# Optimization experiments

Hardware: AMD Instinct MI355X
Metric: run time of the kernel (lower is better)

## Reference

```python
import jax, jax.numpy as jnp
import numpy as np

N = 30000      # nodes
E = 480000     # edges (avg degree 16)
NF = 4         # n_field
NM = 8         # n_meshfield
H = 128        # hidden_size == latent_size
T = 4          # n_time
DEPTH_MID = 8  # depth-2 middle convs per GCNBlock
EPS = 1e-5     # PyG InstanceNorm eps
DT = 5 * (4.0 / 200)  # = 0.1, hard-coded in forward


def _glorot(k, shape):
    fan_in = shape[-2]
    return (jax.random.uniform(k, shape, jnp.float32, -1.0, 1.0) / np.sqrt(fan_in)).astype(jnp.float32)


def setup_inputs() -> dict:
    key = jax.random.key(0)
    ks = jax.random.split(key, 12)
    inp = {}
    inp['F_0'] = jax.random.normal(ks[0], (N, NF), jnp.float32)
    inp['edge_index'] = jax.random.randint(ks[1], (2, E), 0, N)
    inp['meshfield'] = jax.random.normal(ks[2], (N, NM), jnp.float32)
    inp['n_time'] = T
    # mesh_decriptor GCNBlock params (10 GCNConv layers)
    inp['mesh_W0'] = _glorot(ks[3], (NM, H)); inp['mesh_b0'] = jnp.zeros((H,), jnp.float32)
    inp['mesh_Wh'] = _glorot(ks[4], (DEPTH_MID, H, H)); inp['mesh_bh'] = jnp.zeros((DEPTH_MID, H), jnp.float32)
    inp['mesh_W9'] = _glorot(ks[5], (H, H)); inp['mesh_b9'] = jnp.zeros((H,), jnp.float32)
    # differentiator GCNBlock params; input dim = n_field + latent_size
    din = NF + H
    inp['diff_W0'] = _glorot(ks[6], (din, H)); inp['diff_b0'] = jnp.zeros((H,), jnp.float32)
    inp['diff_Wh'] = _glorot(ks[7], (DEPTH_MID, H, H)); inp['diff_bh'] = jnp.zeros((DEPTH_MID, H), jnp.float32)
    inp['diff_W9'] = _glorot(ks[8], (H, NF)); inp['diff_b9'] = jnp.zeros((NF,), jnp.float32)
    return inp


def _gcn_norm(edge_index, n):
    # PyG GCNConv: add self-loops, sym-normalize D^-1/2 (A+I) D^-1/2
    loops = jnp.arange(n)
    row = jnp.concatenate([edge_index[0], loops])
    col = jnp.concatenate([edge_index[1], loops])
    deg = jax.ops.segment_sum(jnp.ones_like(col, jnp.float32), col, num_segments=n)
    dinv = jnp.where(deg > 0, jax.lax.rsqrt(jnp.maximum(deg, 1.0)), 0.0)
    return row, col, dinv[row] * dinv[col]


def _conv(x, W, b, row, col, enorm, n):
    h = x @ W                                   # [n, out]
    m = h[row] * enorm[:, None]                 # gather + edge normalization
    return jax.ops.segment_sum(m, col, num_segments=n) + b  # scatter-add + bias


def _instance_norm(x):
    # single graph, affine=False: per-channel normalize over nodes
    m = x.mean(axis=0)
    v = x.var(axis=0)
    return (x - m) * jax.lax.rsqrt(v + EPS)


def _gcn_block(x, W0, b0, Wh, bh, W9, b9, row, col, enorm, n):
    x = _conv(x, W0, b0, row, col, enorm, n)
    x = _instance_norm(x)
    def body(c, wb):
        W, b = wb
        return _conv(jax.nn.relu(c), W, b, row, col, enorm, n), None
    x, _ = jax.lax.scan(body, x, (Wh, bh))
    return _conv(x, W9, b9, row, col, enorm, n)


def reference(F_0, edge_index, meshfield, n_time,
              mesh_W0, mesh_b0, mesh_Wh, mesh_bh, mesh_W9, mesh_b9,
              diff_W0, diff_b0, diff_Wh, diff_bh, diff_W9, diff_b9):
    n = F_0.shape[0]
    row, col, enorm = _gcn_norm(edge_index, n)
    mesh = jnp.tanh(_gcn_block(meshfield, mesh_W0, mesh_b0, mesh_Wh, mesh_bh,
                               mesh_W9, mesh_b9, row, col, enorm, n))

    def step(F_cur, _):
        x = jnp.concatenate([F_cur, mesh], axis=1)   # [n, n_field + latent]
        F_dot = jnp.tanh(_gcn_block(x, diff_W0, diff_b0, diff_Wh, diff_bh,
                                    diff_W9, diff_b9, row, col, enorm, n))
        F_next = jnp.tanh(F_cur + F_dot * DT)
        # original: F_current = F_next.detach()
        return jax.lax.stop_gradient(F_next), (F_next, F_dot)

    _, (Fs, F_dots) = jax.lax.scan(step, F_0, None, length=n_time)
    # [T, n, f] -> [n, T, f] to match torch.cat(..., dim=1)
    return jnp.transpose(Fs, (1, 0, 2)), jnp.transpose(F_dots, (1, 0, 2))
```

## Files before the change

### kernel.cpp

```cpp
#include <hip/hip_runtime.h>
#include <math.h>

typedef __attribute__((ext_vector_type(8))) short short8;
typedef __attribute__((ext_vector_type(4))) float f32x4;
typedef unsigned int uint;
typedef unsigned short ushort;

__device__ __forceinline__ ushort f2bf(float f) {
  union { float f; uint u; } v; v.f = f;
  uint u = v.u;
  uint r = (u + 0x7FFFu + ((u >> 16) & 1u)) >> 16;
  return (ushort)r;
}
__device__ __forceinline__ float bflo(uint u) { union { uint u; float f; } v; v.u = u << 16; return v.f; }
__device__ __forceinline__ float bfhi(uint u) { union { uint u; float f; } v; v.u = u & 0xFFFF0000u; return v.f; }
__device__ __forceinline__ uint packbf(float a, float b) { return (uint)f2bf(a) | ((uint)f2bf(b) << 16); }


static __global__ void k_count(const int* __restrict__ col, int* __restrict__ cnt, int E) {
  int e = blockIdx.x * blockDim.x + threadIdx.x;
  if (e < E) atomicAdd(&cnt[col[e]], 1);
}

static __global__ void k_dinv(const int* __restrict__ cnt, float* __restrict__ dinv, int N) {
  int v = blockIdx.x * blockDim.x + threadIdx.x;
  if (v < N) dinv[v] = rsqrtf((float)cnt[v] + 1.0f);
}

static __global__ __launch_bounds__(1024) void k_scan(const int* __restrict__ cnt,
                                                      int* __restrict__ rowptr, int N) {
  const int t = threadIdx.x;
  const int per = (N + 1023) / 1024;
  int lo = t * per, hi = min(lo + per, N);
  if (lo > N) lo = N;
  if (hi < lo) hi = lo;
  int sum = 0;
  for (int i = lo; i < hi; ++i) sum += cnt[i];
  int lane = t & 63, w = t >> 6;
  int v = sum;
#pragma unroll
  for (int d = 1; d < 64; d <<= 1) {
    int u = __shfl_up(v, d, 64);
    if (lane >= d) v += u;
  }
  __shared__ int wsum[16];
  if (lane == 63) wsum[w] = v;
  __syncthreads();
  if (t < 16) {
    int x = wsum[t];
#pragma unroll
    for (int d = 1; d < 16; d <<= 1) {
      int u = __shfl_up(x, d, 64);
      if (t >= d) x += u;
    }
    wsum[t] = x;
  }
  __syncthreads();
  int base = (w ? wsum[w - 1] : 0) + v - sum;
  int run = base;
  for (int i = lo; i < hi; ++i) { rowptr[i] = run; run += cnt[i]; }
  if (t == 1023) rowptr[N] = run;
}

static __global__ void k_fill(const int* __restrict__ row, const int* __restrict__ col,
                              const float* __restrict__ dinv, const int* __restrict__ rowptr,
                              int* __restrict__ fillc, int* __restrict__ csr_src,
                              float* __restrict__ csr_w, int E) {
  int e = blockIdx.x * blockDim.x + threadIdx.x;
  if (e >= E) return;
  int s = row[e], d = col[e];
  int pos = rowptr[d] + atomicAdd(&fillc[d], 1);
  csr_src[pos] = s;
  csr_w[pos] = dinv[s] * dinv[d];
}


static __global__ void k_wprep(const float* __restrict__ W, ushort* __restrict__ Wt,
                               int K, int Kpad, int Nc) {
  int l = blockIdx.y;
  int idx = blockIdx.x * 256 + threadIdx.x;
  if (idx >= Nc * Kpad) return;
  int n = idx / Kpad, k = idx - n * Kpad;
  const float* Wl = W + (size_t)l * K * Nc;
  ushort* Wtl = Wt + (size_t)l * Nc * Kpad;
  Wtl[idx] = (k < K) ? f2bf(Wl[(size_t)k * Nc + n]) : (ushort)0;
}


static __global__ __launch_bounds__(256) void k_gemm16(
    const ushort* __restrict__ A, const ushort* __restrict__ Bt,
    int K, const float* __restrict__ bias,
    float* __restrict__ outF, ushort* __restrict__ outB,
    float* __restrict__ statac,
    int M) {
  __shared__ ushort As[128 * 40];
  __shared__ ushort Bs[128 * 40];
  const int tid = threadIdx.x;
  const int lane = tid & 63;
  const int wave = tid >> 6;
  const int wr = wave >> 1, wc = wave & 1;
  const int bm = blockIdx.x * 128;
  const int l15 = lane & 15, lk = lane >> 4;
  const int r0 = tid >> 2, o0 = tid & 3;

  f32x4 acc[4][4];
#pragma unroll
  for (int i = 0; i < 4; ++i)
#pragma unroll
    for (int j = 0; j < 4; ++j) acc[i][j] = (f32x4){0.f, 0.f, 0.f, 0.f};

  for (int k0 = 0; k0 < K; k0 += 32) {
    short8 a0 = *(const short8*)(A + (size_t)(bm + r0) * K + k0 + o0 * 8);
    short8 a1 = *(const short8*)(A + (size_t)(bm + r0 + 64) * K + k0 + o0 * 8);
    short8 b0 = *(const short8*)(Bt + (size_t)r0 * K + k0 + o0 * 8);
    short8 b1 = *(const short8*)(Bt + (size_t)(r0 + 64) * K + k0 + o0 * 8);
    __syncthreads();
    *(short8*)(As + r0 * 40 + o0 * 8) = a0;
    *(short8*)(As + (r0 + 64) * 40 + o0 * 8) = a1;
    *(short8*)(Bs + r0 * 40 + o0 * 8) = b0;
    *(short8*)(Bs + (r0 + 64) * 40 + o0 * 8) = b1;
    __syncthreads();
    short8 af[4], bfr[4];
#pragma unroll
    for (int i = 0; i < 4; ++i) {
      af[i]  = *(const short8*)(As + (wr * 64 + i * 16 + l15) * 40 + lk * 8);
      bfr[i] = *(const short8*)(Bs + (wc * 64 + i * 16 + l15) * 40 + lk * 8);
    }
#pragma unroll
    for (int i = 0; i < 4; ++i)
#pragma unroll
      for (int j = 0; j < 4; ++j)
        acc[i][j] = __builtin_amdgcn_mfma_f32_16x16x32_bf16(af[i], bfr[j], acc[i][j], 0, 0, 0);
  }
#pragma unroll
  for (int i = 0; i < 4; ++i) {
#pragma unroll
    for (int r = 0; r < 4; ++r) {
      int row = bm + wr * 64 + i * 16 + lk * 4 + r;
      if (row >= M) continue;
#pragma unroll
      for (int j = 0; j < 4; ++j) {
        int col = wc * 64 + j * 16 + l15;
        float v = acc[i][j][r] + (bias ? bias[col] : 0.f);
        if (outF) outF[(size_t)row * 128 + col] = v;
        if (outB) outB[(size_t)row * 128 + col] = f2bf(v);
      }
    }
  }
  if (statac) {
    __syncthreads();
    float* sums = (float*)As;
    for (int ii = tid; ii < 256; ii += 256) sums[ii] = 0.f;
    __syncthreads();
#pragma unroll
    for (int j = 0; j < 4; ++j) {
      int col = wc * 64 + j * 16 + l15;
      float s = 0.f, q = 0.f;
#pragma unroll
      for (int i = 0; i < 4; ++i) {
#pragma unroll
        for (int r = 0; r < 4; ++r) {
          int row = bm + wr * 64 + i * 16 + lk * 4 + r;
          if (row < M) {
            float v = acc[i][j][r] + (bias ? bias[col] : 0.f);
            s += v; q += v * v;
          }
        }
      }
      atomicAdd(&sums[col], s);
      atomicAdd(&sums[128 + col], q);
    }
    __syncthreads();
    if (tid < 128) {
      atomicAdd(&statac[tid], sums[tid]);
      atomicAdd(&statac[128 + tid], sums[128 + tid]);
    }
  }
}


static __global__ __launch_bounds__(256) void k_gemm_small(
    const ushort* __restrict__ A, const float* __restrict__ W, float* __restrict__ Y, int M) {
  __shared__ float Ws[512];
  int tid = threadIdx.x;
  for (int i = tid; i < 512; i += 256) Ws[i] = W[i];
  __syncthreads();
  int m = blockIdx.x * 256 + tid;
  if (m >= M) return;
  const uint* a = (const uint*)(A + (size_t)m * 128);
  float a0 = 0, a1 = 0, a2 = 0, a3 = 0;
#pragma unroll 8
  for (int k2 = 0; k2 < 64; ++k2) {
    uint u = a[k2];
    float x0 = bflo(u), x1 = bfhi(u);
    const float* w = Ws + k2 * 8;
    a0 += x0 * w[0] + x1 * w[4];
    a1 += x0 * w[1] + x1 * w[5];
    a2 += x0 * w[2] + x1 * w[6];
    a3 += x0 * w[3] + x1 * w[7];
  }
  float* y = Y + (size_t)m * 4;
  y[0] = a0; y[1] = a1; y[2] = a2; y[3] = a3;
}


static __global__ __launch_bounds__(256) void k_agg16(
    const ushort* __restrict__ Hm, const int* __restrict__ rowptr,
    const int* __restrict__ csr_src, const float* __restrict__ csr_w,
    const float* __restrict__ dinv, const float* __restrict__ bias,
    float* __restrict__ outF,
    ushort* __restrict__ outB, int actB,
    int N) {
  int node = blockIdx.x * 16 + (threadIdx.x >> 4);
  if (node >= N) return;
  int lane = threadIdx.x & 15;
  const uint4* __restrict__ Hq = (const uint4*)Hm;
  float dv = dinv[node];
  float w = dv * dv;
  uint4 su = Hq[(size_t)node * 16 + lane];
  float a0 = w * bflo(su.x), a1 = w * bfhi(su.x);
  float a2 = w * bflo(su.y), a3 = w * bfhi(su.y);
  float a4 = w * bflo(su.z), a5 = w * bfhi(su.z);
  float a6 = w * bflo(su.w), a7 = w * bfhi(su.w);
  int s = rowptr[node], e = rowptr[node + 1];
  int i = s;
  for (; i + 8 <= e; i += 8) {
    int s0 = csr_src[i], s1 = csr_src[i + 1], s2 = csr_src[i + 2], s3 = csr_src[i + 3];
    int s4 = csr_src[i + 4], s5 = csr_src[i + 5], s6 = csr_src[i + 6], s7 = csr_src[i + 7];
    float w0 = csr_w[i], w1 = csr_w[i + 1], w2 = csr_w[i + 2], w3 = csr_w[i + 3];
    float w4 = csr_w[i + 4], w5 = csr_w[i + 5], w6 = csr_w[i + 6], w7 = csr_w[i + 7];
    uint4 u0 = Hq[(size_t)s0 * 16 + lane];
    uint4 u1 = Hq[(size_t)s1 * 16 + lane];
    uint4 u2 = Hq[(size_t)s2 * 16 + lane];
    uint4 u3 = Hq[(size_t)s3 * 16 + lane];
    uint4 u4 = Hq[(size_t)s4 * 16 + lane];
    uint4 u5 = Hq[(size_t)s5 * 16 + lane];
    uint4 u6 = Hq[(size_t)s6 * 16 + lane];
    uint4 u7 = Hq[(size_t)s7 * 16 + lane];
    a0 += w0 * bflo(u0.x) + w1 * bflo(u1.x) + w2 * bflo(u2.x) + w3 * bflo(u3.x)
        + w4 * bflo(u4.x) + w5 * bflo(u5.x) + w6 * bflo(u6.x) + w7 * bflo(u7.x);
    a1 += w0 * bfhi(u0.x) + w1 * bfhi(u1.x) + w2 * bfhi(u2.x) + w3 * bfhi(u3.x)
        + w4 * bfhi(u4.x) + w5 * bfhi(u5.x) + w6 * bfhi(u6.x) + w7 * bfhi(u7.x);
    a2 += w0 * bflo(u0.y) + w1 * bflo(u1.y) + w2 * bflo(u2.y) + w3 * bflo(u3.y)
        + w4 * bflo(u4.y) + w5 * bflo(u5.y) + w6 * bflo(u6.y) + w7 * bflo(u7.y);
    a3 += w0 * bfhi(u0.y) + w1 * bfhi(u1.y) + w2 * bfhi(u2.y) + w3 * bfhi(u3.y)
        + w4 * bfhi(u4.y) + w5 * bfhi(u5.y) + w6 * bfhi(u6.y) + w7 * bfhi(u7.y);
    a4 += w0 * bflo(u0.z) + w1 * bflo(u1.z) + w2 * bflo(u2.z) + w3 * bflo(u3.z)
        + w4 * bflo(u4.z) + w5 * bflo(u5.z) + w6 * bflo(u6.z) + w7 * bflo(u7.z);
    a5 += w0 * bfhi(u0.z) + w1 * bfhi(u1.z) + w2 * bfhi(u2.z) + w3 * bfhi(u3.z)
        + w4 * bfhi(u4.z) + w5 * bfhi(u5.z) + w6 * bfhi(u6.z) + w7 * bfhi(u7.z);
    a6 += w0 * bflo(u0.w) + w1 * bflo(u1.w) + w2 * bflo(u2.w) + w3 * bflo(u3.w)
        + w4 * bflo(u4.w) + w5 * bflo(u5.w) + w6 * bflo(u6.w) + w7 * bflo(u7.w);
    a7 += w0 * bfhi(u0.w) + w1 * bfhi(u1.w) + w2 * bfhi(u2.w) + w3 * bfhi(u3.w)
        + w4 * bfhi(u4.w) + w5 * bfhi(u5.w) + w6 * bfhi(u6.w) + w7 * bfhi(u7.w);
  }
  for (; i < e; ++i) {
    int s0 = csr_src[i];
    float w0 = csr_w[i];
    uint4 u0 = Hq[(size_t)s0 * 16 + lane];
    a0 += w0 * bflo(u0.x); a1 += w0 * bfhi(u0.x);
    a2 += w0 * bflo(u0.y); a3 += w0 * bfhi(u0.y);
    a4 += w0 * bflo(u0.z); a5 += w0 * bfhi(u0.z);
    a6 += w0 * bflo(u0.w); a7 += w0 * bfhi(u0.w);
  }
  if (bias) {
    float4 b0 = *(const float4*)(bias + lane * 8);
    float4 b1 = *(const float4*)(bias + lane * 8 + 4);
    a0 += b0.x; a1 += b0.y; a2 += b0.z; a3 += b0.w;
    a4 += b1.x; a5 += b1.y; a6 += b1.z; a7 += b1.w;
  }
  if (outF) {
    *(float4*)(outF + (size_t)node * 128 + lane * 8)     = make_float4(a0, a1, a2, a3);
    *(float4*)(outF + (size_t)node * 128 + lane * 8 + 4) = make_float4(a4, a5, a6, a7);
  }
  if (outB) {
    float o0 = a0, o1 = a1, o2 = a2, o3 = a3, o4 = a4, o5 = a5, o6 = a6, o7 = a7;
    if (actB == 1) {
      o0 = fmaxf(o0, 0.f); o1 = fmaxf(o1, 0.f); o2 = fmaxf(o2, 0.f); o3 = fmaxf(o3, 0.f);
      o4 = fmaxf(o4, 0.f); o5 = fmaxf(o5, 0.f); o6 = fmaxf(o6, 0.f); o7 = fmaxf(o7, 0.f);
    } else if (actB == 2) {
      o0 = tanhf(o0); o1 = tanhf(o1); o2 = tanhf(o2); o3 = tanhf(o3);
      o4 = tanhf(o4); o5 = tanhf(o5); o6 = tanhf(o6); o7 = tanhf(o7);
    }
    uint4 ov;
    ov.x = packbf(o0, o1); ov.y = packbf(o2, o3);
    ov.z = packbf(o4, o5); ov.w = packbf(o6, o7);
    ((uint4*)outB)[(size_t)node * 16 + lane] = ov;
  }
}


static __global__ void k_aggF(const float* __restrict__ F, const int* __restrict__ rowptr,
                              const int* __restrict__ csr_src, const float* __restrict__ csr_w,
                              const float* __restrict__ dinv, ushort* __restrict__ C160, int N) {
  int idx = blockIdx.x * blockDim.x + threadIdx.x;
  if (idx >= N * 2) return;
  int v = idx >> 1, pr = idx & 1;
  float dv = dinv[v];
  float2 x = *(const float2*)(F + (size_t)v * 4 + pr * 2);
  float a0 = dv * dv * x.x, a1 = dv * dv * x.y;
  int s = rowptr[v], e = rowptr[v + 1];
  for (int i = s; i < e; ++i) {
    float2 xs = *(const float2*)(F + (size_t)csr_src[i] * 4 + pr * 2);
    float w = csr_w[i];
    a0 += w * xs.x;
    a1 += w * xs.y;
  }
  ((uint*)C160)[(size_t)v * 80 + pr] = packbf(a0, a1);
}


static __global__ void k_buildC160(const ushort* __restrict__ AggMesh16,
                                   ushort* __restrict__ C160, int N, int Mpad) {
  int idx = blockIdx.x * blockDim.x + threadIdx.x;
  if (idx >= Mpad * 80) return;
  int v = idx / 80, j = idx - v * 80;
  uint val = 0;
  if (j >= 2 && j < 66 && v < N) val = ((const uint*)AggMesh16)[(size_t)v * 64 + (j - 2)];
  ((uint*)C160)[idx] = val;
}


static __global__ void k_agg_f32(const float* __restrict__ Hm, float* __restrict__ Y,
                                 const int* __restrict__ rowptr, const int* __restrict__ csr_src,
                                 const float* __restrict__ csr_w, const float* __restrict__ dinv,
                                 const float* __restrict__ bias, int N, int C) {
  int idx = blockIdx.x * blockDim.x + threadIdx.x;
  if (idx >= N * C) return;
  int v = idx / C, c = idx - v * C;
  float dv = dinv[v];
  float acc = dv * dv * Hm[(size_t)v * C + c];
  int s = rowptr[v], e = rowptr[v + 1];
  for (int i = s; i < e; ++i) acc += csr_w[i] * Hm[(size_t)csr_src[i] * C + c];
  Y[idx] = acc + bias[c];
}


static __global__ __launch_bounds__(256) void k_in_part(const float* __restrict__ X,
                                                        float* __restrict__ statac, int N) {
  int tid = threadIdx.x;
  int c4 = (tid & 31) * 4;
  int rsub = tid >> 5;
  int row0 = blockIdx.x * 512 + rsub;
  int rowEnd = min(blockIdx.x * 512 + 512, N);
  float s0 = 0, s1 = 0, s2 = 0, s3 = 0, q0 = 0, q1 = 0, q2 = 0, q3 = 0;
  for (int r = row0; r < rowEnd; r += 8) {
    float4 v = *(const float4*)(X + (size_t)r * 128 + c4);
    s0 += v.x; s1 += v.y; s2 += v.z; s3 += v.w;
    q0 += v.x * v.x; q1 += v.y * v.y; q2 += v.z * v.z; q3 += v.w * v.w;
  }
  __shared__ float sb[8][132], qb[8][132];
  sb[rsub][c4] = s0; sb[rsub][c4 + 1] = s1; sb[rsub][c4 + 2] = s2; sb[rsub][c4 + 3] = s3;
  qb[rsub][c4] = q0; qb[rsub][c4 + 1] = q1; qb[rsub][c4 + 2] = q2; qb[rsub][c4 + 3] = q3;
  __syncthreads();
  if (tid < 128) {
    float ss = 0, qq = 0;
#pragma unroll
    for (int g = 0; g < 8; ++g) { ss += sb[g][tid]; qq += qb[g][tid]; }
    atomicAdd(&statac[tid], ss);
    atomicAdd(&statac[128 + tid], qq);
  }
}

static __global__ __launch_bounds__(256) void k_in_apply(const float* __restrict__ X,
                                                         const float* __restrict__ statac,
                                                         ushort* __restrict__ outB, int N) {
  __shared__ float mv[128], sv[128];
  int tid = threadIdx.x;
  if (tid < 128) {
    float m = statac[tid] / (float)N;
    float var = statac[128 + tid] / (float)N - m * m;
    mv[tid] = m;
    sv[tid] = rsqrtf(var + 1e-5f);
  }
  __syncthreads();
  int idx = blockIdx.x * 256 + tid;
  if (idx >= N * 64) return;
  int c2 = idx & 63;
  float2 x = *(const float2*)(X + (size_t)idx * 2);
  float o0 = fmaxf((x.x - mv[c2 * 2]) * sv[c2 * 2], 0.f);
  float o1 = fmaxf((x.y - mv[c2 * 2 + 1]) * sv[c2 * 2 + 1], 0.f);
  ((uint*)outB)[idx] = packbf(o0, o1);
}


static __global__ void k_cast_mesh0(const float* __restrict__ MF, ushort* __restrict__ C32, int N) {
  int idx = blockIdx.x * blockDim.x + threadIdx.x;
  if (idx >= N * 16) return;
  int v = idx >> 4, c2 = idx & 15;
  int c = c2 * 2;
  float x0 = 0.f, x1 = 0.f;
  if (c < 8) { x0 = MF[v * 8 + c]; x1 = MF[v * 8 + c + 1]; }
  ((uint*)C32)[idx] = packbf(x0, x1);
}

static __global__ void k_copy(const float* __restrict__ A, float* __restrict__ B, int n) {
  int i = blockIdx.x * blockDim.x + threadIdx.x;
  if (i < n) B[i] = A[i];
}

static __global__ void k_step_finish(const float* __restrict__ fdot_pre,
                                     const float* __restrict__ Fcur, float* __restrict__ Fnext,
                                     float* __restrict__ out, int N, int T, int t) {
  int idx = blockIdx.x * blockDim.x + threadIdx.x;
  if (idx >= N * 4) return;
  int v = idx >> 2, f = idx & 3;
  float fd = tanhf(fdot_pre[idx]);
  float fn = tanhf(Fcur[idx] + fd * 0.1f);
  Fnext[idx] = fn;
  out[((size_t)v * T + t) * 4 + f] = fn;
  out[(size_t)N * T * 4 + ((size_t)v * T + t) * 4 + f] = fd;
}


extern "C" void kernel_launch(void* const* d_in, const int* in_sizes, int n_in,
                              void* d_out, int out_size, void* d_ws, size_t ws_size,
                              hipStream_t stream) {
  const float* F0        = (const float*)d_in[0];
  const int*   ei        = (const int*)d_in[1];
  const float* meshfield = (const float*)d_in[2];
  const float* mesh_W0 = (const float*)d_in[4];
  const float* mesh_b0 = (const float*)d_in[5];
  const float* mesh_Wh = (const float*)d_in[6];
  const float* mesh_bh = (const float*)d_in[7];
  const float* mesh_W9 = (const float*)d_in[8];
  const float* mesh_b9 = (const float*)d_in[9];
  const float* diff_W0 = (const float*)d_in[10];
  const float* diff_b0 = (const float*)d_in[11];
  const float* diff_Wh = (const float*)d_in[12];
  const float* diff_bh = (const float*)d_in[13];
  const float* diff_W9 = (const float*)d_in[14];
  const float* diff_b9 = (const float*)d_in[15];

  const int N = in_sizes[0] / 4;
  const int E = in_sizes[1] / 2;
  const int H = in_sizes[5];
  const int T = out_size / (N * 4 * 2);
  const int DEPTH = in_sizes[7] / H;
  const int Mpad = (N + 127) / 128 * 128;

  const int* erow = ei;
  const int* ecol = ei + E;

  char* p = (char*)d_ws;
  auto alloc = [&](size_t bytes) { char* r = p; p += (bytes + 255) & ~(size_t)255; return r; };
  float* dinv     = (float*)alloc((size_t)N * 4);
  float* X        = (float*)alloc((size_t)N * H * 4);
  ushort* C32     = (ushort*)alloc((size_t)Mpad * 32 * 2);
  ushort* C160    = (ushort*)alloc((size_t)Mpad * 160 * 2);
  ushort* X16a    = (ushort*)alloc((size_t)Mpad * 128 * 2);
  ushort* X16b    = (ushort*)alloc((size_t)Mpad * 128 * 2);
  ushort* Msg16   = (ushort*)alloc((size_t)Mpad * 128 * 2);
  ushort* meshL16 = (ushort*)alloc((size_t)Mpad * 128 * 2);
  ushort* AggM16  = (ushort*)alloc((size_t)Mpad * 128 * 2);
  float* msg4     = (float*)alloc((size_t)N * 4 * 4);
  float* fdotp    = (float*)alloc((size_t)N * 4 * 4);
  float* fcur0    = (float*)alloc((size_t)N * 4 * 4);
  float* fcur1    = (float*)alloc((size_t)N * 4 * 4);
  float* statac   = (float*)alloc(256 * 4);
  ushort* W0t_m   = (ushort*)alloc((size_t)128 * 32 * 2);
  ushort* Wht_m   = (ushort*)alloc((size_t)DEPTH * 128 * 128 * 2);
  ushort* W9t_m   = (ushort*)alloc((size_t)128 * 128 * 2);
  ushort* W0t_d   = (ushort*)alloc((size_t)128 * 160 * 2);
  ushort* Wht_d   = (ushort*)alloc((size_t)DEPTH * 128 * 128 * 2);
  float* csr_w    = (float*)alloc((size_t)E * 4);
  int* cnt        = (int*)alloc((size_t)N * 4);
  int* rowptr     = (int*)alloc((size_t)(N + 1) * 4);
  int* fillc      = (int*)alloc((size_t)N * 4);
  int* csr_src    = (int*)alloc((size_t)E * 4);

  {
    dim3 g0((128 * 32 + 255) / 256, 1);
    k_wprep<<<g0, 256, 0, stream>>>(mesh_W0, W0t_m, 8, 32, 128);
    dim3 gh((128 * 128 + 255) / 256, DEPTH);
    k_wprep<<<gh, 256, 0, stream>>>(mesh_Wh, Wht_m, 128, 128, 128);
    dim3 g9((128 * 128 + 255) / 256, 1);
    k_wprep<<<g9, 256, 0, stream>>>(mesh_W9, W9t_m, 128, 128, 128);
    dim3 gd((128 * 160 + 255) / 256, 1);
    k_wprep<<<gd, 256, 0, stream>>>(diff_W0, W0t_d, 132, 160, 128);
    k_wprep<<<gh, 256, 0, stream>>>(diff_Wh, Wht_d, 128, 128, 128);
  }

  hipMemsetAsync(cnt, 0, (size_t)N * 4, stream);
  hipMemsetAsync(fillc, 0, (size_t)N * 4, stream);
  k_count<<<(E + 255) / 256, 256, 0, stream>>>(ecol, cnt, E);
  k_dinv<<<(N + 255) / 256, 256, 0, stream>>>(cnt, dinv, N);
  k_scan<<<1, 1024, 0, stream>>>(cnt, rowptr, N);
  k_fill<<<(E + 255) / 256, 256, 0, stream>>>(erow, ecol, dinv, rowptr, fillc, csr_src, csr_w, E);

  auto gemm = [&](const ushort* A, const ushort* Bt, int K, const float* bias,
                  float* oF, ushort* oB, float* st) {
    k_gemm16<<<Mpad / 128, 256, 0, stream>>>(A, Bt, K, bias, oF, oB, st, N);
  };
  auto agg = [&](const ushort* Hm, const float* bias, float* oF, ushort* oB, int actB) {
    k_agg16<<<(N + 15) / 16, 256, 0, stream>>>(Hm, rowptr, csr_src, csr_w, dinv, bias,
                                               oF, oB, actB, N);
  };
  auto in_apply = [&]() {
    k_in_apply<<<(N * 64 + 255) / 256, 256, 0, stream>>>(X, statac, X16a, N);
  };

  k_cast_mesh0<<<(N * 16 + 255) / 256, 256, 0, stream>>>(meshfield, C32, N);
  gemm(C32, W0t_m, 32, nullptr, nullptr, Msg16, nullptr);
  agg(Msg16, mesh_b0, X, nullptr, 0);
  hipMemsetAsync(statac, 0, 256 * 4, stream);
  k_in_part<<<(N + 511) / 512, 256, 0, stream>>>(X, statac, N);
  in_apply();
  {
    ushort* cur = X16a; ushort* nxt = X16b;
    for (int i = 0; i < DEPTH; ++i) {
      gemm(cur, Wht_m + (size_t)i * 128 * 128, 128, nullptr, nullptr, Msg16, nullptr);
      agg(Msg16, mesh_bh + (size_t)i * H, nullptr, nxt, (i < DEPTH - 1) ? 1 : 0);
      ushort* tmp = cur; cur = nxt; nxt = tmp;
    }
    gemm(cur, W9t_m, 128, nullptr, nullptr, Msg16, nullptr);
    agg(Msg16, mesh_b9, nullptr, meshL16, 2 );
  }
  agg(meshL16, nullptr, nullptr, AggM16, 0);
  k_buildC160<<<(Mpad * 80 + 255) / 256, 256, 0, stream>>>(AggM16, C160, N, Mpad);

  k_copy<<<(N * 4 + 255) / 256, 256, 0, stream>>>(F0, fcur0, N * 4);
  float* fc = fcur0;
  float* fn = fcur1;
  float* out = (float*)d_out;

  for (int t = 0; t < T; ++t) {
    k_aggF<<<(N * 2 + 255) / 256, 256, 0, stream>>>(fc, rowptr, csr_src, csr_w, dinv, C160, N);
    hipMemsetAsync(statac, 0, 256 * 4, stream);
    gemm(C160, W0t_d, 160, diff_b0, X, nullptr, statac);
    in_apply();
    ushort* cur = X16a; ushort* nxt = X16b;
    for (int i = 0; i < DEPTH; ++i) {
      gemm(cur, Wht_d + (size_t)i * 128 * 128, 128, nullptr, nullptr, Msg16, nullptr);
      agg(Msg16, diff_bh + (size_t)i * H, nullptr, nxt, (i < DEPTH - 1) ? 1 : 0);
      ushort* tmp = cur; cur = nxt; nxt = tmp;
    }
    k_gemm_small<<<(N + 255) / 256, 256, 0, stream>>>(cur, diff_W9, msg4, N);
    k_agg_f32<<<(N * 4 + 255) / 256, 256, 0, stream>>>(msg4, fdotp, rowptr, csr_src, csr_w,
                                                       dinv, diff_b9, N, 4);
    k_step_finish<<<(N * 4 + 255) / 256, 256, 0, stream>>>(fdotp, fc, fn, out, N, T, t);
    float* tmp = fc; fc = fn; fn = tmp;
  }
}
```

Baseline: 2.232 ms.

## Split GEMM output into two 64-column halves and aggregate each half separately

The GEMM now writes its bf16 message output as two column halves, each stored contiguously as [Mpad,64]. The aggregation kernel launches twice as many blocks, each handling one half for 16 nodes. Blocks are ordered so that the two halves of a group of four node-groups run close together. This halves the per-node gather footprint, aiming for better cache hit rates on the random neighbor gathers, at the cost of duplicated index and weight reads and narrower 8-byte loads. The meshL16 output is written in split layout so it can feed the following aggregation.

```diff
diff --git a/kernel.cpp b/kernel.cpp
--- a/kernel.cpp
+++ b/kernel.cpp
@@ -90,9 +90,10 @@
 static __global__ __launch_bounds__(256) void k_gemm16(
     const ushort* __restrict__ A, const ushort* __restrict__ Bt,
     int K, const float* __restrict__ bias,
-    float* __restrict__ outF, ushort* __restrict__ outB,
+    float* __restrict__ outF,
+    ushort* __restrict__ outB,
     float* __restrict__ statac,
-    int M) {
+    int M, int Mpad) {
   __shared__ ushort As[128 * 40];
   __shared__ ushort Bs[128 * 40];
   const int tid = threadIdx.x;
@@ -132,6 +133,7 @@
       for (int j = 0; j < 4; ++j)
         acc[i][j] = __builtin_amdgcn_mfma_f32_16x16x32_bf16(af[i], bfr[j], acc[i][j], 0, 0, 0);
   }
+  const size_t halfB = (size_t)Mpad * 64;
 #pragma unroll
   for (int i = 0; i < 4; ++i) {
 #pragma unroll
@@ -143,7 +145,7 @@
         int col = wc * 64 + j * 16 + l15;
         float v = acc[i][j][r] + (bias ? bias[col] : 0.f);
         if (outF) outF[(size_t)row * 128 + col] = v;
-        if (outB) outB[(size_t)row * 128 + col] = f2bf(v);
+        if (outB) outB[(size_t)wc * halfB + (size_t)row * 64 + (col & 63)] = f2bf(v);
       }
     }
   }
@@ -209,19 +211,21 @@
     const int* __restrict__ csr_src, const float* __restrict__ csr_w,
     const float* __restrict__ dinv, const float* __restrict__ bias,
     float* __restrict__ outF,
-    ushort* __restrict__ outB, int actB,
-    int N) {
-  int node = blockIdx.x * 16 + (threadIdx.x >> 4);
+    ushort* __restrict__ outB, int actB, int outSplit,
+    int N, int Mpad) {
+  const int G = (N + 15) >> 4;
+  const int g = (blockIdx.x >> 3) * 4 + (blockIdx.x & 3);
+  if (g >= G) return;
+  const int h = (blockIdx.x >> 2) & 1;
+  const int node = g * 16 + (threadIdx.x >> 4);
   if (node >= N) return;
-  int lane = threadIdx.x & 15;
-  const uint4* __restrict__ Hq = (const uint4*)Hm;
+  const int lane = threadIdx.x & 15;
+  const uint2* __restrict__ Hu = (const uint2*)Hm + (size_t)h * Mpad * 16;
   float dv = dinv[node];
   float w = dv * dv;
-  uint4 su = Hq[(size_t)node * 16 + lane];
+  uint2 su = Hu[(size_t)node * 16 + lane];
   float a0 = w * bflo(su.x), a1 = w * bfhi(su.x);
   float a2 = w * bflo(su.y), a3 = w * bfhi(su.y);
-  float a4 = w * bflo(su.z), a5 = w * bfhi(su.z);
-  float a6 = w * bflo(su.w), a7 = w * bfhi(su.w);
   int s = rowptr[node], e = rowptr[node + 1];
   int i = s;
   for (; i + 8 <= e; i += 8) {
@@ -229,14 +233,14 @@
     int s4 = csr_src[i + 4], s5 = csr_src[i + 5], s6 = csr_src[i + 6], s7 = csr_src[i + 7];
     float w0 = csr_w[i], w1 = csr_w[i + 1], w2 = csr_w[i + 2], w3 = csr_w[i + 3];
     float w4 = csr_w[i + 4], w5 = csr_w[i + 5], w6 = csr_w[i + 6], w7 = csr_w[i + 7];
-    uint4 u0 = Hq[(size_t)s0 * 16 + lane];
-    uint4 u1 = Hq[(size_t)s1 * 16 + lane];
-    uint4 u2 = Hq[(size_t)s2 * 16 + lane];
-    uint4 u3 = Hq[(size_t)s3 * 16 + lane];
-    uint4 u4 = Hq[(size_t)s4 * 16 + lane];
-    uint4 u5 = Hq[(size_t)s5 * 16 + lane];
-    uint4 u6 = Hq[(size_t)s6 * 16 + lane];
-    uint4 u7 = Hq[(size_t)s7 * 16 + lane];
+    uint2 u0 = Hu[(size_t)s0 * 16 + lane];
+    uint2 u1 = Hu[(size_t)s1 * 16 + lane];
+    uint2 u2 = Hu[(size_t)s2 * 16 + lane];
+    uint2 u3 = Hu[(size_t)s3 * 16 + lane];
+    uint2 u4 = Hu[(size_t)s4 * 16 + lane];
+    uint2 u5 = Hu[(size_t)s5 * 16 + lane];
+    uint2 u6 = Hu[(size_t)s6 * 16 + lane];
+    uint2 u7 = Hu[(size_t)s7 * 16 + lane];
     a0 += w0 * bflo(u0.x) + w1 * bflo(u1.x) + w2 * bflo(u2.x) + w3 * bflo(u3.x)
         + w4 * bflo(u4.x) + w5 * bflo(u5.x) + w6 * bflo(u6.x) + w7 * bflo(u7.x);
     a1 += w0 * bfhi(u0.x) + w1 * bfhi(u1.x) + w2 * bfhi(u2.x) + w3 * bfhi(u3.x)
@@ -245,47 +249,36 @@
         + w4 * bflo(u4.y) + w5 * bflo(u5.y) + w6 * bflo(u6.y) + w7 * bflo(u7.y);
     a3 += w0 * bfhi(u0.y) + w1 * bfhi(u1.y) + w2 * bfhi(u2.y) + w3 * bfhi(u3.y)
         + w4 * bfhi(u4.y) + w5 * bfhi(u5.y) + w6 * bfhi(u6.y) + w7 * bfhi(u7.y);
-    a4 += w0 * bflo(u0.z) + w1 * bflo(u1.z) + w2 * bflo(u2.z) + w3 * bflo(u3.z)
-        + w4 * bflo(u4.z) + w5 * bflo(u5.z) + w6 * bflo(u6.z) + w7 * bflo(u7.z);
-    a5 += w0 * bfhi(u0.z) + w1 * bfhi(u1.z) + w2 * bfhi(u2.z) + w3 * bfhi(u3.z)
-        + w4 * bfhi(u4.z) + w5 * bfhi(u5.z) + w6 * bfhi(u6.z) + w7 * bfhi(u7.z);
-    a6 += w0 * bflo(u0.w) + w1 * bflo(u1.w) + w2 * bflo(u2.w) + w3 * bflo(u3.w)
-        + w4 * bflo(u4.w) + w5 * bflo(u5.w) + w6 * bflo(u6.w) + w7 * bflo(u7.w);
-    a7 += w0 * bfhi(u0.w) + w1 * bfhi(u1.w) + w2 * bfhi(u2.w) + w3 * bfhi(u3.w)
-        + w4 * bfhi(u4.w) + w5 * bfhi(u5.w) + w6 * bfhi(u6.w) + w7 * bfhi(u7.w);
   }
   for (; i < e; ++i) {
     int s0 = csr_src[i];
     float w0 = csr_w[i];
-    uint4 u0 = Hq[(size_t)s0 * 16 + lane];
+    uint2 u0 = Hu[(size_t)s0 * 16 + lane];
     a0 += w0 * bflo(u0.x); a1 += w0 * bfhi(u0.x);
     a2 += w0 * bflo(u0.y); a3 += w0 * bfhi(u0.y);
-    a4 += w0 * bflo(u0.z); a5 += w0 * bfhi(u0.z);
-    a6 += w0 * bflo(u0.w); a7 += w0 * bfhi(u0.w);
   }
   if (bias) {
-    float4 b0 = *(const float4*)(bias + lane * 8);
-    float4 b1 = *(const float4*)(bias + lane * 8 + 4);
-    a0 += b0.x; a1 += b0.y; a2 += b0.z; a3 += b0.w;
-    a4 += b1.x; a5 += b1.y; a6 += b1.z; a7 += b1.w;
+    float4 bb = *(const float4*)(bias + h * 64 + lane * 4);
+    a0 += bb.x; a1 += bb.y; a2 += bb.z; a3 += bb.w;
   }
   if (outF) {
-    *(float4*)(outF + (size_t)node * 128 + lane * 8)     = make_float4(a0, a1, a2, a3);
-    *(float4*)(outF + (size_t)node * 128 + lane * 8 + 4) = make_float4(a4, a5, a6, a7);
+    *(float4*)(outF + (size_t)node * 128 + h * 64 + lane * 4) = make_float4(a0, a1, a2, a3);
   }
   if (outB) {
-    float o0 = a0, o1 = a1, o2 = a2, o3 = a3, o4 = a4, o5 = a5, o6 = a6, o7 = a7;
+    float o0 = a0, o1 = a1, o2 = a2, o3 = a3;
     if (actB == 1) {
       o0 = fmaxf(o0, 0.f); o1 = fmaxf(o1, 0.f); o2 = fmaxf(o2, 0.f); o3 = fmaxf(o3, 0.f);
-      o4 = fmaxf(o4, 0.f); o5 = fmaxf(o5, 0.f); o6 = fmaxf(o6, 0.f); o7 = fmaxf(o7, 0.f);
     } else if (actB == 2) {
       o0 = tanhf(o0); o1 = tanhf(o1); o2 = tanhf(o2); o3 = tanhf(o3);
-      o4 = tanhf(o4); o5 = tanhf(o5); o6 = tanhf(o6); o7 = tanhf(o7);
-    }
-    uint4 ov;
-    ov.x = packbf(o0, o1); ov.y = packbf(o2, o3);
-    ov.z = packbf(o4, o5); ov.w = packbf(o6, o7);
-    ((uint4*)outB)[(size_t)node * 16 + lane] = ov;
+    }
+    uint2 ov;
+    ov.x = packbf(o0, o1);
+    ov.y = packbf(o2, o3);
+    if (outSplit) {
+      ((uint2*)outB)[(size_t)h * Mpad * 16 + (size_t)node * 16 + lane] = ov;
+    } else {
+      ((uint2*)outB)[(size_t)node * 32 + h * 16 + lane] = ov;
+    }
   }
 }
 
@@ -488,13 +481,15 @@
   k_scan<<<1, 1024, 0, stream>>>(cnt, rowptr, N);
   k_fill<<<(E + 255) / 256, 256, 0, stream>>>(erow, ecol, dinv, rowptr, fillc, csr_src, csr_w, E);
 
+  const int G_AGG = ((N + 15) / 16 + 3) / 4 * 8;
+
   auto gemm = [&](const ushort* A, const ushort* Bt, int K, const float* bias,
                   float* oF, ushort* oB, float* st) {
-    k_gemm16<<<Mpad / 128, 256, 0, stream>>>(A, Bt, K, bias, oF, oB, st, N);
+    k_gemm16<<<Mpad / 128, 256, 0, stream>>>(A, Bt, K, bias, oF, oB, st, N, Mpad);
   };
-  auto agg = [&](const ushort* Hm, const float* bias, float* oF, ushort* oB, int actB) {
-    k_agg16<<<(N + 15) / 16, 256, 0, stream>>>(Hm, rowptr, csr_src, csr_w, dinv, bias,
-                                               oF, oB, actB, N);
+  auto agg = [&](const ushort* Hm, const float* bias, float* oF, ushort* oB, int actB, int oSplit) {
+    k_agg16<<<G_AGG, 256, 0, stream>>>(Hm, rowptr, csr_src, csr_w, dinv, bias,
+                                       oF, oB, actB, oSplit, N, Mpad);
   };
   auto in_apply = [&]() {
     k_in_apply<<<(N * 64 + 255) / 256, 256, 0, stream>>>(X, statac, X16a, N);
@@ -502,7 +497,7 @@
 
   k_cast_mesh0<<<(N * 16 + 255) / 256, 256, 0, stream>>>(meshfield, C32, N);
   gemm(C32, W0t_m, 32, nullptr, nullptr, Msg16, nullptr);
-  agg(Msg16, mesh_b0, X, nullptr, 0);
+  agg(Msg16, mesh_b0, X, nullptr, 0, 0);
   hipMemsetAsync(statac, 0, 256 * 4, stream);
   k_in_part<<<(N + 511) / 512, 256, 0, stream>>>(X, statac, N);
   in_apply();
@@ -510,13 +505,13 @@
     ushort* cur = X16a; ushort* nxt = X16b;
     for (int i = 0; i < DEPTH; ++i) {
       gemm(cur, Wht_m + (size_t)i * 128 * 128, 128, nullptr, nullptr, Msg16, nullptr);
-      agg(Msg16, mesh_bh + (size_t)i * H, nullptr, nxt, (i < DEPTH - 1) ? 1 : 0);
+      agg(Msg16, mesh_bh + (size_t)i * H, nullptr, nxt, (i < DEPTH - 1) ? 1 : 0, 0);
       ushort* tmp = cur; cur = nxt; nxt = tmp;
     }
     gemm(cur, W9t_m, 128, nullptr, nullptr, Msg16, nullptr);
-    agg(Msg16, mesh_b9, nullptr, meshL16, 2 );
-  }
-  agg(meshL16, nullptr, nullptr, AggM16, 0);
+    agg(Msg16, mesh_b9, nullptr, meshL16, 2 , 1 );
+  }
+  agg(meshL16, nullptr, nullptr, AggM16, 0, 0);
   k_buildC160<<<(Mpad * 80 + 255) / 256, 256, 0, stream>>>(AggM16, C160, N, Mpad);
 
   k_copy<<<(N * 4 + 255) / 256, 256, 0, stream>>>(F0, fcur0, N * 4);
@@ -532,7 +527,7 @@
     ushort* cur = X16a; ushort* nxt = X16b;
     for (int i = 0; i < DEPTH; ++i) {
       gemm(cur, Wht_d + (size_t)i * 128 * 128, 128, nullptr, nullptr, Msg16, nullptr);
-      agg(Msg16, diff_bh + (size_t)i * H, nullptr, nxt, (i < DEPTH - 1) ? 1 : 0);
+      agg(Msg16, diff_bh + (size_t)i * H, nullptr, nxt, (i < DEPTH - 1) ? 1 : 0, 0);
       ushort* tmp = cur; cur = nxt; nxt = tmp;
     }
     k_gemm_small<<<(N + 255) / 256, 256, 0, stream>>>(cur, diff_W9, msg4, N);
```

Result: no change. 2.198 ms (-1.5%).
